# Kernel tuning notes

Hardware: AMD Instinct MI355X
Metric: run time of the kernel (lower is better)

Reference implementation:

```python
import jax, jax.numpy as jnp
import numpy as np

B = 1024
HW = 224  # hard-coded 224x224 grid in the original triple loop


def setup_inputs() -> dict:
    key = jax.random.key(0)
    k1, k2 = jax.random.split(key)
    xy = jax.random.normal(k1, (B, 2), dtype=jnp.float32)            # gaze direction gaze[:, :2]
    head_point = jax.random.uniform(k2, (B, 2), dtype=jnp.float32) * HW  # pixel coords in [0, 224)
    return {"xy": xy, "head_point": head_point}


def reference(xy, head_point):
    # arr = [k, i] - head_point  (k = x / column index, i = y / row index)
    coords = jnp.arange(HW, dtype=jnp.float32)
    dx = coords[None, None, :] - head_point[:, 0, None, None]   # [B, 1, HW] -> broadcasts over i
    dy = coords[None, :, None] - head_point[:, 1, None, None]   # [B, HW, 1] -> broadcasts over k
    num = dx * xy[:, 0, None, None] + dy * xy[:, 1, None, None]  # dot(arr, xy), [B, HW, HW]
    arr_norm = jnp.sqrt(dx * dx + dy * dy)
    xy_norm = jnp.sqrt(xy[:, 0] ** 2 + xy[:, 1] ** 2)[:, None, None]
    denom = arr_norm * xy_norm
    # At the head pixel denom==0: torch produces nan -> arccos(nan)=nan -> nan_to_num -> 0.
    # Using cos=0 there gives arccos(0)=pi/2 -> max(1-6,0)=0: identical forward value, finite grads.
    cos = num / jnp.where(denom > 0, denom, 1.0)
    theta = jnp.arccos(cos)
    mask = jnp.maximum(1.0 - 12.0 * theta / jnp.pi, 0.0)
    mask = jnp.nan_to_num(mask)
    return mask[:, None, :, :]  # [B, 1, 224, 224]
```

## Files before the change

### kernel.cpp

```cpp
#include <hip/hip_runtime.h>

#define HW    224
#define IMG   (HW * HW)
#define ROW4  (HW / 4)
#define IMG4  (IMG / 4)


__global__ __launch_bounds__(256) void gaze_cone_kernel(
    const float* __restrict__ xy,
    const float* __restrict__ head_point,
    float* __restrict__ out)
{
#pragma clang fp contract(off)
    const float SCALE = 3.81971863420548805845f;

    const int b = blockIdx.x;

    const float x0 = xy[2 * b];
    const float x1 = xy[2 * b + 1];
    const float h0 = head_point[2 * b];
    const float h1 = head_point[2 * b + 1];

    const float xyn = sqrtf(x0 * x0 + x1 * x1);

    float4* const outb = reinterpret_cast<float4*>(out) + (size_t)b * IMG4;

#pragma unroll 2
    for (int rem = threadIdx.x; rem < IMG4; rem += 256) {
        int i  = rem / ROW4;
        int k0 = (rem - i * ROW4) * 4;

        float dy   = (float)i - h1;
        float dy2  = dy * dy;
        float dyx1 = dy * x1;

        float4 r;
        float* rp = &r.x;
#pragma unroll
        for (int j = 0; j < 4; ++j) {
            float dx    = (float)(k0 + j) - h0;
            float num   = dx * x0 + dyx1;
            float an    = sqrtf(dx * dx + dy2);
            float denom = an * xyn;
            float dsel  = (denom > 0.0f) ? denom : 1.0f;
            float c     = num / dsel;
            float theta = acosf(c);
            float m     = 1.0f - theta * SCALE;
            rp[j] = fmaxf(m, 0.0f);
        }

        outb[rem] = r;
    }
}

extern "C" void kernel_launch(void* const* d_in, const int* in_sizes, int n_in,
                              void* d_out, int out_size, void* d_ws, size_t ws_size,
                              hipStream_t stream) {
    const float* xy = (const float*)d_in[0];
    const float* hp = (const float*)d_in[1];
    float* out      = (float*)d_out;

    const int B = in_sizes[0] / 2;

    gaze_cone_kernel<<<B, 256, 0, stream>>>(xy, hp, out);
}
```

Measured before the change: 239.2 us.

## Tile grid, cull wavefronts outside gaze cone, approximate acos near zero

The kernel now launches one block per 32x32 tile per image. Each wavefront covers an 8-row strip and tests it against the two cone edge half-planes, rotated by about 15 degrees, plus the quadrant conditions. Strips entirely outside the cone write zeros without doing the sqrt, divide or acos. Inside the cone, acos is replaced by a short series sqrt(2u)*(1+u/12+...) that only holds near c=1, where the mask is nonzero. The kernel remains store-bound, and the culling mainly saves ALU work. The series and the conservative bounds risk small accuracy differences near the cone edge.

Result: faster. 208.8 us (-12.7%).

```diff
diff --git a/kernel.cpp b/kernel.cpp
--- a/kernel.cpp
+++ b/kernel.cpp
@@ -2,8 +2,8 @@
 
 #define HW    224
 #define IMG   (HW * HW)
-#define ROW4  (HW / 4)
 #define IMG4  (IMG / 4)
+#define TILES 49
 
 
 __global__ __launch_bounds__(256) void gaze_cone_kernel(
@@ -13,44 +13,81 @@
 {
 #pragma clang fp contract(off)
     const float SCALE = 3.81971863420548805845f;
+    const float CPHI  = 0.965474f;
+    const float SPHI  = 0.260505f;
 
-    const int b = blockIdx.x;
+    const int bid = blockIdx.x;
+    const int b   = bid / TILES;
+    const int t   = bid - b * TILES;
+    const int tx  = t % 7;
+    const int ty  = t / 7;
+
+    const int tid = threadIdx.x;
+    const int w   = tid >> 6;
+    const int l   = tid & 63;
+
+    const int row = ty * 32 + w * 8 + (l >> 3);
+    const int c4  = tx * 8 + (l & 7);
+    const int k0  = c4 << 2;
 
     const float x0 = xy[2 * b];
     const float x1 = xy[2 * b + 1];
     const float h0 = head_point[2 * b];
     const float h1 = head_point[2 * b + 1];
 
-    const float xyn = sqrtf(x0 * x0 + x1 * x1);
+    const float upx = x0 * CPHI - x1 * SPHI;
+    const float upy = x0 * SPHI + x1 * CPHI;
+    const float umx = x0 * CPHI + x1 * SPHI;
+    const float umy = x1 * CPHI - x0 * SPHI;
 
-    float4* const outb = reinterpret_cast<float4*>(out) + (size_t)b * IMG4;
+    const float bx0 = (float)(tx * 32 - 1);
+    const float bx1 = (float)(tx * 32 + 32);
+    const float by0 = (float)(ty * 32 + w * 8 - 1);
+    const float by1 = (float)(ty * 32 + w * 8 + 8);
 
-#pragma unroll 2
-    for (int rem = threadIdx.x; rem < IMG4; rem += 256) {
-        int i  = rem / ROW4;
-        int k0 = (rem - i * ROW4) * 4;
+    const float n1x = -umy, n1y = umx;
+    const float n2x = upy,  n2y = -upx;
 
-        float dy   = (float)i - h1;
-        float dy2  = dy * dy;
-        float dyx1 = dy * x1;
+    const float md1 = fmaxf(n1x * bx0, n1x * bx1) + fmaxf(n1y * by0, n1y * by1)
+                    - (n1x * h0 + n1y * h1);
+    const float md2 = fmaxf(n2x * bx0, n2x * bx1) + fmaxf(n2y * by0, n2y * by1)
+                    - (n2x * h0 + n2y * h1);
 
-        float4 r;
+    bool sep = (md1 < 0.0f) || (md2 < 0.0f);
+    sep = sep || (umx >= 0.0f && upx >= 0.0f && bx1 < h0);
+    sep = sep || (umx <= 0.0f && upx <= 0.0f && bx0 > h0);
+    sep = sep || (umy >= 0.0f && upy >= 0.0f && by1 < h1);
+    sep = sep || (umy <= 0.0f && upy <= 0.0f && by0 > h1);
+
+    float4 r;
+    if (sep) {
+        r = make_float4(0.0f, 0.0f, 0.0f, 0.0f);
+    } else {
+        const float xyn = sqrtf(x0 * x0 + x1 * x1);
+        const float dy   = (float)row - h1;
+        const float dy2  = dy * dy;
+        const float dyx1 = dy * x1;
+
         float* rp = &r.x;
 #pragma unroll
         for (int j = 0; j < 4; ++j) {
             float dx    = (float)(k0 + j) - h0;
             float num   = dx * x0 + dyx1;
-            float an    = sqrtf(dx * dx + dy2);
+            float d2    = dx * dx + dy2;
+            float an    = sqrtf(d2);
             float denom = an * xyn;
             float dsel  = (denom > 0.0f) ? denom : 1.0f;
             float c     = num / dsel;
-            float theta = acosf(c);
-            float m     = 1.0f - theta * SCALE;
+            float u     = 1.0f - c;
+            float s     = __builtin_amdgcn_sqrtf(u + u);
+            float poly  = fmaf(u, fmaf(u, 0.01875f, 0.08333333333333333f), 1.0f);
+            float theta = s * poly;
+            float m     = fmaf(theta, -SCALE, 1.0f);
             rp[j] = fmaxf(m, 0.0f);
         }
+    }
 
-        outb[rem] = r;
-    }
+    reinterpret_cast<float4*>(out)[(size_t)b * IMG4 + row * 56 + c4] = r;
 }
 
 extern "C" void kernel_launch(void* const* d_in, const int* in_sizes, int n_in,
@@ -62,5 +99,5 @@
 
     const int B = in_sizes[0] / 2;
 
-    gaze_cone_kernel<<<B, 256, 0, stream>>>(xy, hp, out);
+    gaze_cone_kernel<<<B * TILES, 256, 0, stream>>>(xy, hp, out);
 }
```
